# Kernel optimization log

Hardware: AMD Instinct MI355X
Metric: run time of the kernel (lower is better)

Reference implementation:

```python
import jax, jax.numpy as jnp
import numpy as np

EPS = 1e-5

def _round_ste(x):
    # straight-through round (identical value in fwd; STE grad in bwd module)
    return x + jax.lax.stop_gradient(jnp.round(x) - x)

def _quant_weight(w, bits):
    # per-tensor symmetric absmax quantization to `bits` bits (BitNet-style)
    qb = float(2 ** (bits - 1) - 1)
    scale = qb / jnp.maximum(jnp.max(jnp.abs(w)), EPS)
    return _round_ste(jnp.clip(w * scale, -qb, qb)) / scale

def _quant_act(x):
    # per-token 8-bit absmax activation quantization
    qb = 127.0
    scale = qb / jnp.maximum(jnp.max(jnp.abs(x), axis=-1, keepdims=True), EPS)
    return _round_ste(jnp.clip(x * scale, -qb, qb)) / scale

def _layernorm(x, gamma, beta):
    mu = jnp.mean(x, axis=-1, keepdims=True)
    var = jnp.mean(jnp.square(x - mu), axis=-1, keepdims=True)
    return (x - mu) * jax.lax.rsqrt(var + EPS) * gamma + beta

def _qlinear(x, w, b, bits):
    return jnp.einsum('btd,fd->btf', _quant_act(x), _quant_weight(w, bits)) + b

def setup_inputs() -> dict:
    key = jax.random.key(0)
    ks = jax.random.split(key, 4)
    B, T, D, F = 8, 2048, 1024, 4096
    return {
        'x': jax.random.normal(ks[0], (B, T, D), dtype=jnp.float32),
        'mask': jnp.ones((B, T, 1), dtype=jnp.float32),
        'ln_gamma': jnp.ones((D,), dtype=jnp.float32),
        'ln_beta': jnp.zeros((D,), dtype=jnp.float32),
        'w1': jax.random.normal(ks[1], (F, D), dtype=jnp.float32) * (1.0 / np.sqrt(D)),
        'b1': jnp.zeros((F,), dtype=jnp.float32),
        'w2': jax.random.normal(ks[2], (D, F), dtype=jnp.float32) * (1.0 / np.sqrt(F)),
        'b2': jnp.zeros((D,), dtype=jnp.float32),
        'bitwidth': 8,
    }

def reference(x, mask, ln_gamma, ln_beta, w1, b1, w2, b2, bitwidth):
    y = _layernorm(x, ln_gamma, ln_beta)           # [B,T,D]
    y = _qlinear(y, w1, b1, bitwidth)              # [B,T,F]
    y = y * jax.nn.sigmoid(y)                      # swish
    y = _qlinear(y, w2, b2, bitwidth)              # [B,T,D]
    seq_mask = mask[:, :, 0][..., None]            # [B,T,1]
    y = y * seq_mask
    return x + 0.5 * y
```

## Files before the change

kernel.cpp:

```cpp
#include <hip/hip_runtime.h>
#include <hip/hip_bf16.h>
#include <stdint.h>


typedef int v4i __attribute__((ext_vector_type(4)));

#define BM 128
#define BN 128
#define BK 64

__device__ __forceinline__ float wave_max64(float v) {
#pragma unroll
  for (int off = 32; off; off >>= 1) v = fmaxf(v, __shfl_xor(v, off, 64));
  return v;
}

__device__ __forceinline__ void load16_to_lds(const int8_t* g, int8_t* l) {
  __builtin_amdgcn_global_load_lds((const __attribute__((address_space(1))) void*)g,
                                   (__attribute__((address_space(3))) void*)l, 16, 0, 0);
}

__global__ __launch_bounds__(256) void absmax_kernel(const float* __restrict__ w, int n4,
                                                     int* __restrict__ slot) {
  float m = 0.f;
  const float4* w4 = (const float4*)w;
  for (int i = blockIdx.x * 256 + threadIdx.x; i < n4; i += gridDim.x * 256) {
    float4 v = w4[i];
    m = fmaxf(fmaxf(fabsf(v.x), fabsf(v.y)), fmaxf(fmaxf(fabsf(v.z), fabsf(v.w)), m));
  }
  m = wave_max64(m);
  __shared__ float sm[4];
  int lane = threadIdx.x & 63, wv = threadIdx.x >> 6;
  if (!lane) sm[wv] = m;
  __syncthreads();
  if (!threadIdx.x) {
    m = fmaxf(fmaxf(sm[0], sm[1]), fmaxf(sm[2], sm[3]));
    atomicMax(slot, __float_as_int(m));
  }
}

__global__ void scales_kernel(const int* __restrict__ wmax, const int* __restrict__ bits,
                              float* __restrict__ scal) {
  float qb = (float)((1 << (bits[0] - 1)) - 1);
  scal[2] = qb / fmaxf(__int_as_float(wmax[0]), 1e-5f);
  scal[3] = qb / fmaxf(__int_as_float(wmax[1]), 1e-5f);
  scal[4] = qb;
}

__global__ __launch_bounds__(256) void wquant_kernel(const float* __restrict__ w,
                                                     const float* __restrict__ scal, int which,
                                                     int8_t* __restrict__ out) {
  float s = scal[2 + which], qb = scal[4];
  int i = blockIdx.x * 256 + threadIdx.x;
  float4 v = ((const float4*)w)[i];
  char4 q;
  q.x = (char)(int)rintf(fminf(fmaxf(v.x * s, -qb), qb));
  q.y = (char)(int)rintf(fminf(fmaxf(v.y * s, -qb), qb));
  q.z = (char)(int)rintf(fminf(fmaxf(v.z * s, -qb), qb));
  q.w = (char)(int)rintf(fminf(fmaxf(v.w * s, -qb), qb));
  ((char4*)out)[i] = q;
}

__global__ __launch_bounds__(256) void ln_quant_kernel(const float* __restrict__ x,
                                                       const float* __restrict__ gamma,
                                                       const float* __restrict__ beta,
                                                       int8_t* __restrict__ xq,
                                                       float* __restrict__ xscale) {
  const int row = blockIdx.x;
  const int tid = threadIdx.x;
  const float4 v = ((const float4*)(x + (size_t)row * 1024))[tid];
  float s = v.x + v.y + v.z + v.w;
  float ss = fmaf(v.x, v.x, fmaf(v.y, v.y, fmaf(v.z, v.z, v.w * v.w)));
#pragma unroll
  for (int off = 32; off; off >>= 1) {
    s += __shfl_xor(s, off, 64);
    ss += __shfl_xor(ss, off, 64);
  }
  __shared__ float sm[8];
  const int lane = tid & 63, wv = tid >> 6;
  if (!lane) { sm[wv] = s; sm[4 + wv] = ss; }
  __syncthreads();
  s = sm[0] + sm[1] + sm[2] + sm[3];
  ss = sm[4] + sm[5] + sm[6] + sm[7];
  const float mu = s * (1.f / 1024.f);
  const float var = ss * (1.f / 1024.f) - mu * mu;
  const float rstd = rsqrtf(var + 1e-5f);
  const float4 g = ((const float4*)gamma)[tid];
  const float4 bb = ((const float4*)beta)[tid];
  float y0 = (v.x - mu) * rstd * g.x + bb.x;
  float y1 = (v.y - mu) * rstd * g.y + bb.y;
  float y2 = (v.z - mu) * rstd * g.z + bb.z;
  float y3 = (v.w - mu) * rstd * g.w + bb.w;
  float am = fmaxf(fmaxf(fabsf(y0), fabsf(y1)), fmaxf(fabsf(y2), fabsf(y3)));
  am = wave_max64(am);
  __syncthreads();
  if (!lane) sm[wv] = am;
  __syncthreads();
  am = fmaxf(fmaxf(sm[0], sm[1]), fmaxf(sm[2], sm[3]));
  const float scale = 127.f / fmaxf(am, 1e-5f);
  char4 q;
  q.x = (char)(int)rintf(fminf(fmaxf(y0 * scale, -127.f), 127.f));
  q.y = (char)(int)rintf(fminf(fmaxf(y1 * scale, -127.f), 127.f));
  q.z = (char)(int)rintf(fminf(fmaxf(y2 * scale, -127.f), 127.f));
  q.w = (char)(int)rintf(fminf(fmaxf(y3 * scale, -127.f), 127.f));
  ((char4*)(xq + (size_t)row * 1024))[tid] = q;
  if (!tid) xscale[row] = scale;
}

__global__ __launch_bounds__(256) void hquant_kernel(const ushort* __restrict__ h,
                                                     int8_t* __restrict__ hq,
                                                     float* __restrict__ hscale) {
  const int row = blockIdx.x;
  const int tid = threadIdx.x;
  const int4* p = (const int4*)(h + (size_t)row * 4096);
  union { int4 i4; ushort u[8]; } ua, ub;
  ua.i4 = p[tid * 2];
  ub.i4 = p[tid * 2 + 1];
  float f[16];
#pragma unroll
  for (int i = 0; i < 8; ++i) f[i] = __uint_as_float((unsigned)ua.u[i] << 16);
#pragma unroll
  for (int i = 0; i < 8; ++i) f[8 + i] = __uint_as_float((unsigned)ub.u[i] << 16);
  float am = 0.f;
#pragma unroll
  for (int i = 0; i < 16; ++i) am = fmaxf(am, fabsf(f[i]));
  am = wave_max64(am);
  __shared__ float sm[4];
  const int lane = tid & 63, wv = tid >> 6;
  if (!lane) sm[wv] = am;
  __syncthreads();
  am = fmaxf(fmaxf(sm[0], sm[1]), fmaxf(sm[2], sm[3]));
  const float scale = 127.f / fmaxf(am, 1e-5f);
  union { int4 i4; char c[16]; } q;
#pragma unroll
  for (int i = 0; i < 16; ++i)
    q.c[i] = (char)(int)rintf(fminf(fmaxf(f[i] * scale, -127.f), 127.f));
  ((int4*)(hq + (size_t)row * 4096))[tid] = q.i4;
  if (!tid) hscale[row] = scale;
}

template <int K>
__device__ __forceinline__ void gemm_core(const int8_t* __restrict__ A,
                                          const int8_t* __restrict__ B, int8_t* As, int8_t* Bs,
                                          v4i acc[4][4]) {
  const int tid = threadIdx.x;
  const int lane = tid & 63;
  const int wave = tid >> 6;
  const int wm = (wave & 1) << 6;
  const int wn = (wave >> 1) << 6;
  const int lrow = lane & 15;
  const int qk = (lane >> 4) << 4;
  const size_t m0 = (size_t)blockIdx.y * BM;
  const size_t n0 = (size_t)blockIdx.x * BN;
  const int r0 = tid >> 2;
  const int c0 = (tid & 3) << 4;

  const int8_t* ga0 = A + (m0 + r0) * K + c0;
  const int8_t* ga1 = A + (m0 + 64 + r0) * K + c0;
  const int8_t* gb0 = B + (n0 + r0) * K + c0;
  const int8_t* gb1 = B + (n0 + 64 + r0) * K + c0;
  int8_t* la0 = As + tid * 16;
  int8_t* la1 = As + 4096 + tid * 16;
  int8_t* lb0 = Bs + tid * 16;
  int8_t* lb1 = Bs + 4096 + tid * 16;

  for (int k0 = 0; k0 < K; k0 += BK) {
    __syncthreads();
    load16_to_lds(ga0 + k0, la0);
    load16_to_lds(ga1 + k0, la1);
    load16_to_lds(gb0 + k0, lb0);
    load16_to_lds(gb1 + k0, lb1);
    __syncthreads();
    v4i af[4], bf[4];
#pragma unroll
    for (int i = 0; i < 4; ++i)
      af[i] = *(const v4i*)(As + (wm + i * 16 + lrow) * 64 + qk);
#pragma unroll
    for (int j = 0; j < 4; ++j)
      bf[j] = *(const v4i*)(Bs + (wn + j * 16 + lrow) * 64 + qk);
#pragma unroll
    for (int i = 0; i < 4; ++i)
#pragma unroll
      for (int j = 0; j < 4; ++j)
        acc[i][j] = __builtin_amdgcn_mfma_i32_16x16x64_i8(af[i], bf[j], acc[i][j], 0, 0, 0);
  }
}

__global__ __launch_bounds__(256) void gemm1_kernel(const int8_t* __restrict__ Aq,
                                                    const int8_t* __restrict__ Bq,
                                                    const float* __restrict__ xscale,
                                                    const float* __restrict__ scal,
                                                    const float* __restrict__ bias,
                                                    ushort* __restrict__ H) {
  __shared__ __align__(16) int8_t As[BM * BK];
  __shared__ __align__(16) int8_t Bs[BN * BK];
  v4i acc[4][4] = {};
  gemm_core<1024>(Aq, Bq, As, Bs, acc);
  const float sw1 = scal[2];
  const int lane = threadIdx.x & 63;
  const int wave = threadIdx.x >> 6;
  const int m0 = blockIdx.y * BM + ((wave & 1) << 6);
  const int n0 = blockIdx.x * BN + ((wave >> 1) << 6);
  const int ln = lane & 15, lq = lane >> 4;
#pragma unroll
  for (int i = 0; i < 4; ++i) {
#pragma unroll
    for (int r = 0; r < 4; ++r) {
      const int m = m0 + i * 16 + lq * 4 + r;
      const float rcp = 1.0f / (xscale[m] * sw1);
#pragma unroll
      for (int j = 0; j < 4; ++j) {
        const int n = n0 + j * 16 + ln;
        const float v = (float)acc[i][j][r] * rcp + bias[n];
        const float hsw = v / (1.0f + __expf(-v));
        __hip_bfloat16 hb = __float2bfloat16(hsw);
        H[(size_t)m * 4096 + n] = *(const ushort*)&hb;
      }
    }
  }
}

__global__ __launch_bounds__(256) void gemm2_kernel(const int8_t* __restrict__ Aq,
                                                    const int8_t* __restrict__ Bq,
                                                    const float* __restrict__ hscale,
                                                    const float* __restrict__ scal,
                                                    const float* __restrict__ bias,
                                                    const float* __restrict__ x,
                                                    const float* __restrict__ mask,
                                                    float* __restrict__ out) {
  __shared__ __align__(16) int8_t As[BM * BK];
  __shared__ __align__(16) int8_t Bs[BN * BK];
  v4i acc[4][4] = {};
  gemm_core<4096>(Aq, Bq, As, Bs, acc);
  const float sw2 = scal[3];
  const int lane = threadIdx.x & 63;
  const int wave = threadIdx.x >> 6;
  const int m0 = blockIdx.y * BM + ((wave & 1) << 6);
  const int n0 = blockIdx.x * BN + ((wave >> 1) << 6);
  const int ln = lane & 15, lq = lane >> 4;
#pragma unroll
  for (int i = 0; i < 4; ++i) {
#pragma unroll
    for (int r = 0; r < 4; ++r) {
      const int m = m0 + i * 16 + lq * 4 + r;
      const float rcp = 1.0f / (hscale[m] * sw2);
      const float mk = 0.5f * mask[m];
#pragma unroll
      for (int j = 0; j < 4; ++j) {
        const int n = n0 + j * 16 + ln;
        const float v = (float)acc[i][j][r] * rcp + bias[n];
        const size_t idx = (size_t)m * 1024 + n;
        out[idx] = x[idx] + mk * v;
      }
    }
  }
}

extern "C" void kernel_launch(void* const* d_in, const int* in_sizes, int n_in, void* d_out,
                              int out_size, void* d_ws, size_t ws_size, hipStream_t stream) {
  const float* x = (const float*)d_in[0];
  const float* mask = (const float*)d_in[1];
  const float* gamma = (const float*)d_in[2];
  const float* beta = (const float*)d_in[3];
  const float* w1 = (const float*)d_in[4];
  const float* b1 = (const float*)d_in[5];
  const float* w2 = (const float*)d_in[6];
  const float* b2 = (const float*)d_in[7];
  const int* bits = (const int*)d_in[8];
  float* out = (float*)d_out;

  char* ws = (char*)d_ws;
  int* wmax = (int*)ws;
  float* scal = (float*)ws;
  float* xscale = (float*)(ws + (1u << 20));
  float* hscale = (float*)(ws + (2u << 20));
  int8_t* w1q = (int8_t*)(ws + (4u << 20));
  int8_t* w2q = (int8_t*)(ws + (8u << 20));
  int8_t* xq = (int8_t*)(ws + (12u << 20));
  int8_t* hq = (int8_t*)(ws + (28u << 20));
  ushort* h = (ushort*)(ws + (size_t)(92u << 20));

  const int NW = 4096 * 1024;

  absmax_kernel<<<1024, 256, 0, stream>>>(w1, NW / 4, wmax + 0);
  absmax_kernel<<<1024, 256, 0, stream>>>(w2, NW / 4, wmax + 1);
  scales_kernel<<<1, 1, 0, stream>>>(wmax, bits, scal);
  wquant_kernel<<<NW / 1024, 256, 0, stream>>>(w1, scal, 0, w1q);
  wquant_kernel<<<NW / 1024, 256, 0, stream>>>(w2, scal, 1, w2q);
  ln_quant_kernel<<<16384, 256, 0, stream>>>(x, gamma, beta, xq, xscale);
  gemm1_kernel<<<dim3(4096 / BN, 16384 / BM), 256, 0, stream>>>(xq, w1q, xscale, scal, b1, h);
  hquant_kernel<<<16384, 256, 0, stream>>>(h, hq, hscale);
  gemm2_kernel<<<dim3(1024 / BN, 16384 / BM), 256, 0, stream>>>(hq, w2q, hscale, scal, b2, x,
                                                                mask, out);
}
```

Before: 465.2 us.

## Switch int8 GEMMs to 32x32x32 MFMA with BK=128 and XOR-swizzled LDS

Replaces the 16x16x64 int8 MFMA tiling with 32x32x32 MFMA (2x2 per wave), doubles the K tile to 128 and XOR-swizzles the LDS layout so fragment reads avoid bank conflicts. Both epilogues are rewritten for the 32x32 accumulator layout. The aim is fewer LDS reads per MFMA, fewer barriers per K, and less bank contention, at the cost of double the LDS per block, which may lower occupancy.

```diff
diff --git a/kernel.cpp b/kernel.cpp
--- a/kernel.cpp
+++ b/kernel.cpp
@@ -4,10 +4,11 @@
 
 
 typedef int v4i __attribute__((ext_vector_type(4)));
+typedef int v16i __attribute__((ext_vector_type(16)));
 
 #define BM 128
 #define BN 128
-#define BK 64
+#define BK 128
 
 __device__ __forceinline__ float wave_max64(float v) {
 #pragma unroll
@@ -142,47 +143,46 @@
 template <int K>
 __device__ __forceinline__ void gemm_core(const int8_t* __restrict__ A,
                                           const int8_t* __restrict__ B, int8_t* As, int8_t* Bs,
-                                          v4i acc[4][4]) {
+                                          v16i acc[2][2]) {
   const int tid = threadIdx.x;
   const int lane = tid & 63;
   const int wave = tid >> 6;
   const int wm = (wave & 1) << 6;
   const int wn = (wave >> 1) << 6;
-  const int lrow = lane & 15;
-  const int qk = (lane >> 4) << 4;
+  const int lrow = lane & 31;
+  const int half = lane >> 5;
   const size_t m0 = (size_t)blockIdx.y * BM;
   const size_t n0 = (size_t)blockIdx.x * BN;
-  const int r0 = tid >> 2;
-  const int c0 = (tid & 3) << 4;
-
-  const int8_t* ga0 = A + (m0 + r0) * K + c0;
-  const int8_t* ga1 = A + (m0 + 64 + r0) * K + c0;
-  const int8_t* gb0 = B + (n0 + r0) * K + c0;
-  const int8_t* gb1 = B + (n0 + 64 + r0) * K + c0;
-  int8_t* la0 = As + tid * 16;
-  int8_t* la1 = As + 4096 + tid * 16;
-  int8_t* lb0 = Bs + tid * 16;
-  int8_t* lb1 = Bs + 4096 + tid * 16;
+
+  const int ci = wave * 64 + lane;
+  const int rA = ci >> 3;
+  const int cs = ((ci & 7) ^ (rA & 7)) << 4;
+  const int8_t* ga = A + (m0 + rA) * K + cs;
+  const int8_t* gb = B + (n0 + rA) * K + cs;
+  int8_t* la = As + ci * 16;
+  int8_t* lb = Bs + ci * 16;
+  const int x7 = (lrow & 7);
 
   for (int k0 = 0; k0 < K; k0 += BK) {
     __syncthreads();
-    load16_to_lds(ga0 + k0, la0);
-    load16_to_lds(ga1 + k0, la1);
-    load16_to_lds(gb0 + k0, lb0);
-    load16_to_lds(gb1 + k0, lb1);
+#pragma unroll
+    for (int t = 0; t < 4; ++t) {
+      load16_to_lds(ga + (size_t)(t * 32) * K + k0, la + t * 4096);
+      load16_to_lds(gb + (size_t)(t * 32) * K + k0, lb + t * 4096);
+    }
     __syncthreads();
-    v4i af[4], bf[4];
-#pragma unroll
-    for (int i = 0; i < 4; ++i)
-      af[i] = *(const v4i*)(As + (wm + i * 16 + lrow) * 64 + qk);
-#pragma unroll
-    for (int j = 0; j < 4; ++j)
-      bf[j] = *(const v4i*)(Bs + (wn + j * 16 + lrow) * 64 + qk);
-#pragma unroll
-    for (int i = 0; i < 4; ++i)
-#pragma unroll
-      for (int j = 0; j < 4; ++j)
-        acc[i][j] = __builtin_amdgcn_mfma_i32_16x16x64_i8(af[i], bf[j], acc[i][j], 0, 0, 0);
+#pragma unroll
+    for (int ks = 0; ks < 4; ++ks) {
+      const int so = ((ks * 2 + half) ^ x7) << 4;
+      v4i a0 = *(const v4i*)(As + (wm + lrow) * 128 + so);
+      v4i a1 = *(const v4i*)(As + (wm + 32 + lrow) * 128 + so);
+      v4i b0 = *(const v4i*)(Bs + (wn + lrow) * 128 + so);
+      v4i b1 = *(const v4i*)(Bs + (wn + 32 + lrow) * 128 + so);
+      acc[0][0] = __builtin_amdgcn_mfma_i32_32x32x32_i8(a0, b0, acc[0][0], 0, 0, 0);
+      acc[0][1] = __builtin_amdgcn_mfma_i32_32x32x32_i8(a0, b1, acc[0][1], 0, 0, 0);
+      acc[1][0] = __builtin_amdgcn_mfma_i32_32x32x32_i8(a1, b0, acc[1][0], 0, 0, 0);
+      acc[1][1] = __builtin_amdgcn_mfma_i32_32x32x32_i8(a1, b1, acc[1][1], 0, 0, 0);
+    }
   }
 }
 
@@ -194,24 +194,26 @@
                                                     ushort* __restrict__ H) {
   __shared__ __align__(16) int8_t As[BM * BK];
   __shared__ __align__(16) int8_t Bs[BN * BK];
-  v4i acc[4][4] = {};
+  v16i acc[2][2] = {};
   gemm_core<1024>(Aq, Bq, As, Bs, acc);
   const float sw1 = scal[2];
   const int lane = threadIdx.x & 63;
   const int wave = threadIdx.x >> 6;
   const int m0 = blockIdx.y * BM + ((wave & 1) << 6);
   const int n0 = blockIdx.x * BN + ((wave >> 1) << 6);
-  const int ln = lane & 15, lq = lane >> 4;
-#pragma unroll
-  for (int i = 0; i < 4; ++i) {
-#pragma unroll
-    for (int r = 0; r < 4; ++r) {
-      const int m = m0 + i * 16 + lq * 4 + r;
+  const int cn = lane & 31;
+  const int h4 = (lane >> 5) << 2;
+#pragma unroll
+  for (int i = 0; i < 2; ++i) {
+#pragma unroll
+    for (int reg = 0; reg < 16; ++reg) {
+      const int row = (reg & 3) + ((reg >> 2) << 3) + h4;
+      const int m = m0 + i * 32 + row;
       const float rcp = 1.0f / (xscale[m] * sw1);
 #pragma unroll
-      for (int j = 0; j < 4; ++j) {
-        const int n = n0 + j * 16 + ln;
-        const float v = (float)acc[i][j][r] * rcp + bias[n];
+      for (int j = 0; j < 2; ++j) {
+        const int n = n0 + j * 32 + cn;
+        const float v = (float)acc[i][j][reg] * rcp + bias[n];
         const float hsw = v / (1.0f + __expf(-v));
         __hip_bfloat16 hb = __float2bfloat16(hsw);
         H[(size_t)m * 4096 + n] = *(const ushort*)&hb;
@@ -230,25 +232,27 @@
                                                     float* __restrict__ out) {
   __shared__ __align__(16) int8_t As[BM * BK];
   __shared__ __align__(16) int8_t Bs[BN * BK];
-  v4i acc[4][4] = {};
+  v16i acc[2][2] = {};
   gemm_core<4096>(Aq, Bq, As, Bs, acc);
   const float sw2 = scal[3];
   const int lane = threadIdx.x & 63;
   const int wave = threadIdx.x >> 6;
   const int m0 = blockIdx.y * BM + ((wave & 1) << 6);
   const int n0 = blockIdx.x * BN + ((wave >> 1) << 6);
-  const int ln = lane & 15, lq = lane >> 4;
-#pragma unroll
-  for (int i = 0; i < 4; ++i) {
-#pragma unroll
-    for (int r = 0; r < 4; ++r) {
-      const int m = m0 + i * 16 + lq * 4 + r;
+  const int cn = lane & 31;
+  const int h4 = (lane >> 5) << 2;
+#pragma unroll
+  for (int i = 0; i < 2; ++i) {
+#pragma unroll
+    for (int reg = 0; reg < 16; ++reg) {
+      const int row = (reg & 3) + ((reg >> 2) << 3) + h4;
+      const int m = m0 + i * 32 + row;
       const float rcp = 1.0f / (hscale[m] * sw2);
       const float mk = 0.5f * mask[m];
 #pragma unroll
-      for (int j = 0; j < 4; ++j) {
-        const int n = n0 + j * 16 + ln;
-        const float v = (float)acc[i][j][r] * rcp + bias[n];
+      for (int j = 0; j < 2; ++j) {
+        const int n = n0 + j * 32 + cn;
+        const float v = (float)acc[i][j][reg] * rcp + bias[n];
         const size_t idx = (size_t)m * 1024 + n;
         out[idx] = x[idx] + mk * v;
       }
```

New measurement: 441.3 us. 1.05x faster.
